# Kernel tuning notes

Hardware: AMD Instinct MI355X
Metric: run time of the kernel (lower is better)

## Reference

```python
import jax, jax.numpy as jnp
import numpy as np

# Static graph-batch configuration (equal-size graphs so per-graph top-k is static)
B = 256          # number of graphs in the batch
N = 400          # nodes per graph
D = 256          # in_dim
DEG = 32         # average degree
E = B * N * DEG  # total edges
RATIO = 0.5
K = int(np.ceil(RATIO * N))  # nodes kept per graph by mytopk
NT = B * N


def setup_inputs() -> dict:
    key = jax.random.key(0)
    k1, k2, k3, k4 = jax.random.split(key, 4)
    feature = jax.random.normal(k1, (NT, D), dtype=jnp.float32)
    W = jax.random.normal(k2, (D, 1), dtype=jnp.float32) * (1.0 / np.sqrt(D))
    b = jnp.zeros((1,), dtype=jnp.float32)
    # edges stay within each graph: global id = graph_offset + local id
    g = jnp.repeat(jnp.arange(B, dtype=jnp.int32), N * DEG)  # [E] graph id per edge
    src = g * N + jax.random.randint(k3, (E,), 0, N, dtype=jnp.int32)
    dst = g * N + jax.random.randint(k4, (E,), 0, N, dtype=jnp.int32)
    return {"feature": feature, "W": W, "b": b, "src": src, "dst": dst}


def _forward(feature, W, b, src, dst):
    # --- GraphConv(in_dim, 1), norm='both' (dgl): h = D_in^-1/2 A D_out^-1/2 (X W) + b
    ones_e = jnp.ones((E,), dtype=feature.dtype)
    deg_out = jax.ops.segment_sum(ones_e, src, num_segments=NT)
    deg_in = jax.ops.segment_sum(ones_e, dst, num_segments=NT)
    norm_out = jnp.maximum(deg_out, 1.0) ** -0.5  # dgl clamps degree to min 1
    norm_in = jnp.maximum(deg_in, 1.0) ** -0.5
    h = (feature @ W) * norm_out[:, None]                      # [NT,1]
    agg = jax.ops.segment_sum(h[src], dst, num_segments=NT)    # [NT,1]
    score = (agg * norm_in[:, None] + b)[:, 0]                 # [NT]

    # --- mytopk: per-graph top-k node selection by score (descending)
    score2d = score.reshape(B, N)
    _, idx = jax.lax.top_k(score2d, K)                         # [B,K] local ids
    offsets = (jnp.arange(B, dtype=jnp.int32) * N)[:, None]
    perm = (idx.astype(jnp.int32) + offsets).reshape(-1)       # [B*K] global ids

    # complement nodes (mask trick in the original): ascending order per graph
    sel = jnp.zeros((NT,), dtype=bool).at[perm].set(True)
    sel2d = sel.reshape(B, N).astype(jnp.int32)
    order = jnp.argsort(sel2d, axis=1, stable=True)[:, : N - K]  # unselected first
    perm_com = (order.astype(jnp.int32) + offsets).reshape(-1)   # [B*(N-K)]

    # --- gated feature gathers
    feature_dis = feature[perm] * jnp.tanh(score[perm])[:, None]
    feature_com = feature[perm_com] * jnp.tanh(score[perm_com])[:, None]

    # --- subgraph structure as static-shape edge masks (dgl.node_subgraph keeps
    #     edges whose both endpoints are selected)
    e_dis_mask = sel[src] & sel[dst]
    e_com_mask = (~sel[src]) & (~sel[dst])

    score_soft = jax.nn.softmax(score, axis=0)  # Softmax(dim=0) over all nodes
    return feature_dis, feature_com, perm, perm_com, score_soft, e_dis_mask, e_com_mask


def reference(feature, W, b, src, dst):
    return _forward(feature, W, b, src, dst)
```

## Files before the change

kernel.cpp:

```cpp
#include <hip/hip_runtime.h>
#include <math.h>

#define B_    256
#define N_    400
#define D_    256
#define EPG_  12800
#define E_    3276800
#define NT_   102400
#define K_    200
#define NKC_  200

#define O_FDIS 0
#define O_FCOM 13107200
#define O_PERM 26214400
#define O_PCOM 26265600
#define O_SOFT 26316800
#define O_EDIS 26419200
#define O_ECOM 29696000

#define NEG_INF (-3.402823466e38f)

typedef float nfv4 __attribute__((ext_vector_type(4)));

static __device__ __forceinline__ void nt_store4(float4* p, float4 v) {
    nfv4 x; x.x = v.x; x.y = v.y; x.z = v.z; x.w = v.w;
    __builtin_nontemporal_store(x, (nfv4*)p);
}

__global__ __launch_bounds__(256) void k_h(const float* __restrict__ feat,
                                           const float* __restrict__ W,
                                           float* __restrict__ hraw) {
    const int gw   = (blockIdx.x * 256 + threadIdx.x) >> 6;
    const int lane = threadIdx.x & 63;
    const float4 w4 = ((const float4*)W)[lane];
    const int r0 = gw * 4;
    const float4* fb = (const float4*)feat;
    float4 a0 = fb[(size_t)(r0    ) * 64 + lane];
    float4 a1 = fb[(size_t)(r0 + 1) * 64 + lane];
    float4 a2 = fb[(size_t)(r0 + 2) * 64 + lane];
    float4 a3 = fb[(size_t)(r0 + 3) * 64 + lane];
    float d0 = a0.x*w4.x + a0.y*w4.y + a0.z*w4.z + a0.w*w4.w;
    float d1 = a1.x*w4.x + a1.y*w4.y + a1.z*w4.z + a1.w*w4.w;
    float d2 = a2.x*w4.x + a2.y*w4.y + a2.z*w4.z + a2.w*w4.w;
    float d3 = a3.x*w4.x + a3.y*w4.y + a3.z*w4.z + a3.w*w4.w;
    #pragma unroll
    for (int off = 32; off > 0; off >>= 1) {
        d0 += __shfl_down(d0, off, 64);
        d1 += __shfl_down(d1, off, 64);
        d2 += __shfl_down(d2, off, 64);
        d3 += __shfl_down(d3, off, 64);
    }
    if (lane == 0) {
        hraw[r0    ] = d0;
        hraw[r0 + 1] = d1;
        hraw[r0 + 2] = d2;
        hraw[r0 + 3] = d3;
    }
}

__global__ __launch_bounds__(1024) void k_graph(const int* __restrict__ src,
                                                const int* __restrict__ dst,
                                                const float* __restrict__ hraw,
                                                const float* __restrict__ bp,
                                                float* __restrict__ score,
                                                float* __restrict__ pm,
                                                float* __restrict__ ps,
                                                int* __restrict__ sel,
                                                int* __restrict__ orow,
                                                float* __restrict__ out) {
    __shared__ float hl[N_], scl[N_];
    __shared__ int   ho[N_], hi[N_];
    __shared__ unsigned long long bmask[7];

    const int g = blockIdx.x, tid = threadIdx.x;
    const int nbase = g * N_, ebase = g * EPG_;
    const int wave = tid >> 6, lane = tid & 63;

    float hr = 0.0f;
    if (tid < N_) hr = hraw[nbase + tid];

    if (tid < N_) { ho[tid] = 0; hi[tid] = 0; scl[tid] = 0.0f; }
    __syncthreads();

    const int4* s4 = (const int4*)(src + ebase);
    const int4* d4 = (const int4*)(dst + ebase);

    for (int i = tid; i < EPG_ / 4; i += 1024) {
        int4 s = s4[i]; int4 d = d4[i];
        atomicAdd(&ho[s.x - nbase], 1);
        atomicAdd(&ho[s.y - nbase], 1);
        atomicAdd(&ho[s.z - nbase], 1);
        atomicAdd(&ho[s.w - nbase], 1);
        atomicAdd(&hi[d.x - nbase], 1);
        atomicAdd(&hi[d.y - nbase], 1);
        atomicAdd(&hi[d.z - nbase], 1);
        atomicAdd(&hi[d.w - nbase], 1);
    }
    __syncthreads();

    if (tid < N_)
        hl[tid] = hr * (1.0f / sqrtf(fmaxf((float)ho[tid], 1.0f)));
    __syncthreads();

    for (int i = tid; i < EPG_ / 4; i += 1024) {
        int4 s = s4[i]; int4 d = d4[i];
        atomicAdd(&scl[d.x - nbase], hl[s.x - nbase]);
        atomicAdd(&scl[d.y - nbase], hl[s.y - nbase]);
        atomicAdd(&scl[d.z - nbase], hl[s.z - nbase]);
        atomicAdd(&scl[d.w - nbase], hl[s.w - nbase]);
    }
    __syncthreads();

    const float bb = bp[0];
    if (tid < N_) {
        float v = scl[tid] * (1.0f / sqrtf(fmaxf((float)hi[tid], 1.0f))) + bb;
        scl[tid] = v;
        score[nbase + tid] = v;
    }
    __syncthreads();

    bool selb = false;
    if (tid < 448) {
        float sreg[7];
        #pragma unroll
        for (int t = 0; t < 7; ++t) {
            const int j = t * 64 + lane;
            sreg[t] = (j < N_) ? scl[j] : NEG_INF;
        }
        const float v = (tid < N_) ? scl[tid] : NEG_INF;
        int rnk = 0;
        #pragma unroll
        for (int t = 0; t < 7; ++t) {
            #pragma unroll
            for (int l2 = 0; l2 < 64; ++l2) {
                const float u = __shfl(sreg[t], l2, 64);
                const int j = t * 64 + l2;
                rnk += ((u > v) || (u == v && j < tid)) ? 1 : 0;
            }
        }
        selb = (tid < N_) && (rnk < K_);
        if (tid < N_) sel[nbase + tid] = selb ? 1 : 0;
        if (selb) {
            orow[nbase + tid] = g * K_ + rnk;
            out[O_PERM + g * K_ + rnk] = (float)(nbase + tid);
        }
        unsigned long long bal = __ballot(selb);
        if (lane == 0) bmask[wave] = bal;
    }
    if (wave == 15) {
        float m = NEG_INF;
        for (int i = lane; i < N_; i += 64) m = fmaxf(m, scl[i]);
        #pragma unroll
        for (int o = 32; o > 0; o >>= 1) m = fmaxf(m, __shfl_xor(m, o, 64));
        float s = 0.0f;
        for (int i = lane; i < N_; i += 64) s += expf(scl[i] - m);
        #pragma unroll
        for (int o = 32; o > 0; o >>= 1) s += __shfl_xor(s, o, 64);
        if (lane == 0) { pm[g] = m; ps[g] = s; }
    }
    __syncthreads();

    if (tid < N_ && !selb) {
        int nsel = 0;
        #pragma unroll
        for (int w = 0; w < 7; ++w)
            if (w < wave) nsel += (int)__popcll(bmask[w]);
        nsel += (int)__popcll(bmask[wave] & ((1ull << lane) - 1ull));
        const int pos = tid - nsel;
        orow[nbase + tid] = B_ * K_ + g * NKC_ + pos;
        out[O_PCOM + g * NKC_ + pos] = (float)(nbase + tid);
    }
}

__global__ __launch_bounds__(256) void k_soft_comb(const float* pm, const float* ps, float* red2) {
    __shared__ float rm[256], rs[256];
    int tid = threadIdx.x;
    float m = pm[tid];
    rm[tid] = m; __syncthreads();
    for (int o = 128; o > 0; o >>= 1) { if (tid < o) rm[tid] = fmaxf(rm[tid], rm[tid + o]); __syncthreads(); }
    float M = rm[0]; __syncthreads();
    rs[tid] = ps[tid] * expf(m - M); __syncthreads();
    for (int o = 128; o > 0; o >>= 1) { if (tid < o) rs[tid] += rs[tid + o]; __syncthreads(); }
    if (tid == 0) { red2[0] = M; red2[1] = rs[0]; }
}

__global__ __launch_bounds__(256) void k_mask(const int* __restrict__ src,
                                              const int* __restrict__ dst,
                                              const int* __restrict__ sel,
                                              float* __restrict__ out) {
    const int i = blockIdx.x * 256 + threadIdx.x;
    int4 s = ((const int4*)src)[i];
    int4 d = ((const int4*)dst)[i];
    int a0 = sel[s.x], a1 = sel[s.y], a2 = sel[s.z], a3 = sel[s.w];
    int b0 = sel[d.x], b1 = sel[d.y], b2 = sel[d.z], b3 = sel[d.w];
    float4 mdis, mcom;
    mdis.x = (a0 & b0) ? 1.0f : 0.0f;  mcom.x = (a0 | b0) ? 0.0f : 1.0f;
    mdis.y = (a1 & b1) ? 1.0f : 0.0f;  mcom.y = (a1 | b1) ? 0.0f : 1.0f;
    mdis.z = (a2 & b2) ? 1.0f : 0.0f;  mcom.z = (a2 | b2) ? 0.0f : 1.0f;
    mdis.w = (a3 & b3) ? 1.0f : 0.0f;  mcom.w = (a3 | b3) ? 0.0f : 1.0f;
    nt_store4(((float4*)(out + O_EDIS)) + i, mdis);
    nt_store4(((float4*)(out + O_ECOM)) + i, mcom);
}

__global__ __launch_bounds__(256) void k_gather(const float* __restrict__ feat,
                                                const float* __restrict__ score,
                                                const int* __restrict__ orow,
                                                const float* __restrict__ red2,
                                                float* __restrict__ out) {
    const int gw   = (blockIdx.x * 256 + threadIdx.x) >> 6;
    const int lane = threadIdx.x & 63;
    const int n0 = gw * 4;
    const float4* fb = (const float4*)feat;
    float4 v0 = fb[(size_t)(n0    ) * 64 + lane];
    float4 v1 = fb[(size_t)(n0 + 1) * 64 + lane];
    float4 v2 = fb[(size_t)(n0 + 2) * 64 + lane];
    float4 v3 = fb[(size_t)(n0 + 3) * 64 + lane];
    float s0 = score[n0], s1 = score[n0 + 1], s2 = score[n0 + 2], s3 = score[n0 + 3];
    int   r0 = orow[n0],  r1 = orow[n0 + 1],  r2 = orow[n0 + 2],  r3 = orow[n0 + 3];
    float t0 = tanhf(s0), t1 = tanhf(s1), t2 = tanhf(s2), t3 = tanhf(s3);
    v0.x *= t0; v0.y *= t0; v0.z *= t0; v0.w *= t0;
    v1.x *= t1; v1.y *= t1; v1.z *= t1; v1.w *= t1;
    v2.x *= t2; v2.y *= t2; v2.z *= t2; v2.w *= t2;
    v3.x *= t3; v3.y *= t3; v3.z *= t3; v3.w *= t3;
    nt_store4(((float4*)(out + (size_t)r0 * D_)) + lane, v0);
    nt_store4(((float4*)(out + (size_t)r1 * D_)) + lane, v1);
    nt_store4(((float4*)(out + (size_t)r2 * D_)) + lane, v2);
    nt_store4(((float4*)(out + (size_t)r3 * D_)) + lane, v3);
    if (lane == 0) {
        float M = red2[0], S = red2[1];
        out[O_SOFT + n0    ] = expf(s0 - M) / S;
        out[O_SOFT + n0 + 1] = expf(s1 - M) / S;
        out[O_SOFT + n0 + 2] = expf(s2 - M) / S;
        out[O_SOFT + n0 + 3] = expf(s3 - M) / S;
    }
}

extern "C" void kernel_launch(void* const* d_in, const int* in_sizes, int n_in,
                              void* d_out, int out_size, void* d_ws, size_t ws_size,
                              hipStream_t stream) {
    const float* feat = (const float*)d_in[0];
    const float* W    = (const float*)d_in[1];
    const float* bp   = (const float*)d_in[2];
    const int*   src  = (const int*)d_in[3];
    const int*   dst  = (const int*)d_in[4];
    float* out = (float*)d_out;

    char* ws = (char*)d_ws;
    float* hraw  = (float*)(ws + 0);
    float* score = (float*)(ws + 409600);
    int*   sel   = (int*)  (ws + 819200);
    int*   orow  = (int*)  (ws + 1228800);
    float* pm    = (float*)(ws + 1638400);
    float* ps    = (float*)(ws + 1639424);
    float* red2  = (float*)(ws + 1640448);

    k_h        <<<NT_ / 16,    256, 0, stream>>>(feat, W, hraw);
    k_graph    <<<B_,         1024, 0, stream>>>(src, dst, hraw, bp,
                                                 score, pm, ps, sel, orow, out);
    k_soft_comb<<<1,           256, 0, stream>>>(pm, ps, red2);
    k_mask     <<<E_ / 4 / 256, 256, 0, stream>>>(src, dst, sel, out);
    k_gather   <<<NT_ / 16,    256, 0, stream>>>(feat, score, orow, red2, out);
}
```

Baseline: 294.0 us.

## Split per-graph kernel into degree, scatter and top-k kernels across more blocks

The single 256-block kernel that did degree counting, edge aggregation and top-k is split into three kernels. Degree and scatter now run on 4 blocks per graph, using per-wave privatized shared histograms that are merged into global memory with atomics. The top-k rank loop uses readlane and skips out-of-range lanes. The intent is to fill the GPU better than 256 large blocks could, at the cost of two extra launches, global atomics and reusing workspace buffers through aliasing.

```diff
diff --git a/kernel.cpp b/kernel.cpp
--- a/kernel.cpp
+++ b/kernel.cpp
@@ -21,7 +21,6 @@
 #define NEG_INF (-3.402823466e38f)
 
 typedef float nfv4 __attribute__((ext_vector_type(4)));
-
 static __device__ __forceinline__ void nt_store4(float4* p, float4 v) {
     nfv4 x; x.x = v.x; x.y = v.y; x.z = v.z; x.w = v.w;
     __builtin_nontemporal_store(x, (nfv4*)p);
@@ -29,8 +28,11 @@
 
 __global__ __launch_bounds__(256) void k_h(const float* __restrict__ feat,
                                            const float* __restrict__ W,
-                                           float* __restrict__ hraw) {
-    const int gw   = (blockIdx.x * 256 + threadIdx.x) >> 6;
+                                           float* __restrict__ hraw,
+                                           int* __restrict__ degz) {
+    const int gid  = blockIdx.x * 256 + threadIdx.x;
+    if (gid < 2 * NT_) degz[gid] = 0;
+    const int gw   = gid >> 6;
     const int lane = threadIdx.x & 63;
     const float4 w4 = ((const float4*)W)[lane];
     const int r0 = gw * 4;
@@ -58,64 +60,89 @@
     }
 }
 
-__global__ __launch_bounds__(1024) void k_graph(const int* __restrict__ src,
-                                                const int* __restrict__ dst,
-                                                const float* __restrict__ hraw,
-                                                const float* __restrict__ bp,
-                                                float* __restrict__ score,
-                                                float* __restrict__ pm,
-                                                float* __restrict__ ps,
-                                                int* __restrict__ sel,
-                                                int* __restrict__ orow,
-                                                float* __restrict__ out) {
-    __shared__ float hl[N_], scl[N_];
-    __shared__ int   ho[N_], hi[N_];
+__global__ __launch_bounds__(256) void k_deg(const int* __restrict__ src,
+                                             const int* __restrict__ dst,
+                                             int* __restrict__ dego,
+                                             int* __restrict__ degi,
+                                             float* __restrict__ aggz) {
+    __shared__ int hp[8][N_];
+    const int blk = blockIdx.x, tid = threadIdx.x, wave = tid >> 6;
+    const int gid = blk * 256 + tid;
+    if (gid < NT_) aggz[gid] = 0.0f;
+    for (int t = tid; t < 8 * N_; t += 256) ((int*)hp)[t] = 0;
+    __syncthreads();
+
+    const int g = blk >> 2, nbase = g * N_;
+    int* hw_o = hp[wave * 2 + 0];
+    int* hw_i = hp[wave * 2 + 1];
+    const int4* s4 = (const int4*)(src + blk * (EPG_ / 4));
+    const int4* d4 = (const int4*)(dst + blk * (EPG_ / 4));
+    for (int i = tid; i < EPG_ / 16; i += 256) {
+        int4 s = s4[i]; int4 d = d4[i];
+        atomicAdd(&hw_o[s.x - nbase], 1);
+        atomicAdd(&hw_o[s.y - nbase], 1);
+        atomicAdd(&hw_o[s.z - nbase], 1);
+        atomicAdd(&hw_o[s.w - nbase], 1);
+        atomicAdd(&hw_i[d.x - nbase], 1);
+        atomicAdd(&hw_i[d.y - nbase], 1);
+        atomicAdd(&hw_i[d.z - nbase], 1);
+        atomicAdd(&hw_i[d.w - nbase], 1);
+    }
+    __syncthreads();
+    for (int t = tid; t < N_; t += 256) {
+        atomicAdd(&dego[nbase + t], hp[0][t] + hp[2][t] + hp[4][t] + hp[6][t]);
+        atomicAdd(&degi[nbase + t], hp[1][t] + hp[3][t] + hp[5][t] + hp[7][t]);
+    }
+}
+
+__global__ __launch_bounds__(256) void k_scat(const int* __restrict__ src,
+                                              const int* __restrict__ dst,
+                                              const float* __restrict__ hraw,
+                                              const int* __restrict__ dego,
+                                              float* __restrict__ agg) {
+    __shared__ float hl[N_];
+    __shared__ float sp[4][N_];
+    const int blk = blockIdx.x, tid = threadIdx.x, wave = tid >> 6;
+    const int g = blk >> 2, nbase = g * N_;
+    for (int t = tid; t < N_; t += 256)
+        hl[t] = hraw[nbase + t] * (1.0f / sqrtf(fmaxf((float)dego[nbase + t], 1.0f)));
+    for (int t = tid; t < 4 * N_; t += 256) ((float*)sp)[t] = 0.0f;
+    __syncthreads();
+
+    float* spw = sp[wave];
+    const int4* s4 = (const int4*)(src + blk * (EPG_ / 4));
+    const int4* d4 = (const int4*)(dst + blk * (EPG_ / 4));
+    for (int i = tid; i < EPG_ / 16; i += 256) {
+        int4 s = s4[i]; int4 d = d4[i];
+        atomicAdd(&spw[d.x - nbase], hl[s.x - nbase]);
+        atomicAdd(&spw[d.y - nbase], hl[s.y - nbase]);
+        atomicAdd(&spw[d.z - nbase], hl[s.z - nbase]);
+        atomicAdd(&spw[d.w - nbase], hl[s.w - nbase]);
+    }
+    __syncthreads();
+    for (int t = tid; t < N_; t += 256)
+        atomicAdd(&agg[nbase + t], sp[0][t] + sp[1][t] + sp[2][t] + sp[3][t]);
+}
+
+__global__ __launch_bounds__(512) void k_top(float* __restrict__ sc,
+                                             const int* __restrict__ degi,
+                                             const float* __restrict__ bp,
+                                             float* __restrict__ pm,
+                                             float* __restrict__ ps,
+                                             int* __restrict__ sel,
+                                             int* __restrict__ orow,
+                                             float* __restrict__ out) {
+    __shared__ float scl[N_];
     __shared__ unsigned long long bmask[7];
-
     const int g = blockIdx.x, tid = threadIdx.x;
-    const int nbase = g * N_, ebase = g * EPG_;
     const int wave = tid >> 6, lane = tid & 63;
-
-    float hr = 0.0f;
-    if (tid < N_) hr = hraw[nbase + tid];
-
-    if (tid < N_) { ho[tid] = 0; hi[tid] = 0; scl[tid] = 0.0f; }
-    __syncthreads();
-
-    const int4* s4 = (const int4*)(src + ebase);
-    const int4* d4 = (const int4*)(dst + ebase);
-
-    for (int i = tid; i < EPG_ / 4; i += 1024) {
-        int4 s = s4[i]; int4 d = d4[i];
-        atomicAdd(&ho[s.x - nbase], 1);
-        atomicAdd(&ho[s.y - nbase], 1);
-        atomicAdd(&ho[s.z - nbase], 1);
-        atomicAdd(&ho[s.w - nbase], 1);
-        atomicAdd(&hi[d.x - nbase], 1);
-        atomicAdd(&hi[d.y - nbase], 1);
-        atomicAdd(&hi[d.z - nbase], 1);
-        atomicAdd(&hi[d.w - nbase], 1);
-    }
-    __syncthreads();
-
-    if (tid < N_)
-        hl[tid] = hr * (1.0f / sqrtf(fmaxf((float)ho[tid], 1.0f)));
-    __syncthreads();
-
-    for (int i = tid; i < EPG_ / 4; i += 1024) {
-        int4 s = s4[i]; int4 d = d4[i];
-        atomicAdd(&scl[d.x - nbase], hl[s.x - nbase]);
-        atomicAdd(&scl[d.y - nbase], hl[s.y - nbase]);
-        atomicAdd(&scl[d.z - nbase], hl[s.z - nbase]);
-        atomicAdd(&scl[d.w - nbase], hl[s.w - nbase]);
-    }
-    __syncthreads();
+    const int nbase = g * N_;
 
     const float bb = bp[0];
     if (tid < N_) {
-        float v = scl[tid] * (1.0f / sqrtf(fmaxf((float)hi[tid], 1.0f))) + bb;
+        float v = sc[nbase + tid] * (1.0f / sqrtf(fmaxf((float)degi[nbase + tid], 1.0f))) + bb;
+        sc[nbase + tid] = v;
         scl[tid] = v;
-        score[nbase + tid] = v;
     }
     __syncthreads();
 
@@ -133,9 +160,12 @@
         for (int t = 0; t < 7; ++t) {
             #pragma unroll
             for (int l2 = 0; l2 < 64; ++l2) {
-                const float u = __shfl(sreg[t], l2, 64);
                 const int j = t * 64 + l2;
-                rnk += ((u > v) || (u == v && j < tid)) ? 1 : 0;
+                if (j < N_) {
+                    const float u = __uint_as_float(
+                        __builtin_amdgcn_readlane(__float_as_uint(sreg[t]), l2));
+                    rnk += ((u > v) || (u == v && j < tid)) ? 1 : 0;
+                }
             }
         }
         selb = (tid < N_) && (rnk < K_);
@@ -147,7 +177,7 @@
         unsigned long long bal = __ballot(selb);
         if (lane == 0) bmask[wave] = bal;
     }
-    if (wave == 15) {
+    if (wave == 7) {
         float m = NEG_INF;
         for (int i = lane; i < N_; i += 64) m = fmaxf(m, scl[i]);
         #pragma unroll
@@ -246,18 +276,22 @@
     float* out = (float*)d_out;
 
     char* ws = (char*)d_ws;
-    float* hraw  = (float*)(ws + 0);
-    float* score = (float*)(ws + 409600);
-    int*   sel   = (int*)  (ws + 819200);
-    int*   orow  = (int*)  (ws + 1228800);
+    int*   dego  = (int*)  (ws + 0);
+    int*   degi  = (int*)  (ws + 409600);
+    float* agg   = (float*)(ws + 819200);
+    float* hraw  = (float*)(ws + 1228800);
     float* pm    = (float*)(ws + 1638400);
     float* ps    = (float*)(ws + 1639424);
     float* red2  = (float*)(ws + 1640448);
-
-    k_h        <<<NT_ / 16,    256, 0, stream>>>(feat, W, hraw);
-    k_graph    <<<B_,         1024, 0, stream>>>(src, dst, hraw, bp,
-                                                 score, pm, ps, sel, orow, out);
-    k_soft_comb<<<1,           256, 0, stream>>>(pm, ps, red2);
+    int*   orow  = (int*)  (ws + 0);
+    int*   sel   = (int*)  (ws + 1228800);
+    float* score = agg;
+
+    k_h        <<<NT_ / 16,     256, 0, stream>>>(feat, W, hraw, dego);
+    k_deg      <<<4 * B_,       256, 0, stream>>>(src, dst, dego, degi, agg);
+    k_scat     <<<4 * B_,       256, 0, stream>>>(src, dst, hraw, dego, agg);
+    k_top      <<<B_,           512, 0, stream>>>(score, degi, bp, pm, ps, sel, orow, out);
+    k_soft_comb<<<1,            256, 0, stream>>>(pm, ps, red2);
     k_mask     <<<E_ / 4 / 256, 256, 0, stream>>>(src, dst, sel, out);
-    k_gather   <<<NT_ / 16,    256, 0, stream>>>(feat, score, orow, red2, out);
-}
+    k_gather   <<<NT_ / 16,     256, 0, stream>>>(feat, score, orow, red2, out);
+}
```

New measurement: 293.8 us. No clear change (-0.1%).
